# Kernel optimization log

Measured on AMD Instinct MI355X. Metric: run time of the kernel, lower is better.

## Reference

```python
import jax, jax.numpy as jnp
import numpy as np

B, N, C = 4, 4096, 512
K = 683  # ceil(N / ratio=6.0)
TAU = 1.0
W_OCC, W_REP, W_ENT = 1.0, 0.1, 0.01
REP_TOPK, REP_MARGIN = 4, -1.0
NEG = -1e9


def setup_inputs() -> dict:
    key = jax.random.key(0)
    ks = jax.random.split(key, 5)
    s = jax.random.normal(ks[0], (B, N, C), jnp.float32)
    mu = jax.random.normal(ks[1], (B, N, 3), jnp.float32)
    # SPD covariance per residue: L L^T + 0.1 I
    L = jax.random.normal(ks[2], (B, N, 3, 3), jnp.float32) * 0.3
    Sigma = jnp.einsum('bnij,bnkj->bnik', L, L) + 0.1 * jnp.eye(3, dtype=jnp.float32)
    mask = jnp.ones((B, N), jnp.float32)
    W = jax.random.normal(ks[3], (C, C), jnp.float32) / np.sqrt(C).astype(np.float32)
    b = jnp.zeros((C,), jnp.float32)
    slots = jax.random.normal(ks[4], (K, C), jnp.float32) * 0.02
    return {"s": s, "mu": mu, "Sigma": Sigma, "mask": mask, "W": W, "b": b, "slots": slots}


def reference(s, mu, Sigma, mask, W, b, slots):
    Kk = slots.shape[0]
    # A = softmax((Linear(s)) . slots / tau), masked
    s_proj = jnp.einsum('bnc,dc->bnd', s, W) + b            # nn.Linear: x @ W^T + b
    logits = jnp.einsum('bnc,kc->bnk', s_proj, slots) / TAU
    logits = jnp.where((mask < 0.5)[..., None], NEG, logits)
    A = jax.nn.softmax(logits, axis=-1) * mask[..., None]   # [B,N,K]

    denom = jnp.maximum(A.sum(axis=1), 1e-8)                # [B,K]
    s_c = jnp.einsum('bnk,bnc->bkc', A, s) / denom[..., None]

    # moment-matching merge
    w = A / (A.sum(axis=1, keepdims=True) + 1e-8)           # [B,N,K]
    mu_c = jnp.einsum('bnk,bnd->bkd', w, mu)                # [B,K,3]
    intra = jnp.einsum('bnk,bnij->bkij', w, Sigma)          # [B,K,3,3]
    diff = mu[:, :, None, :] - mu_c[:, None, :, :]          # [B,N,K,3]
    inter = jnp.einsum('bnk,bnki,bnkj->bkij', w, diff, diff)
    Sigma_c = intra + inter                                 # [B,K,3,3]

    # occupancy balance loss
    occ = A.sum(axis=1)
    occ = occ / jnp.maximum(occ.sum(axis=-1, keepdims=True), 1e-8)
    loss_occ = jnp.mean((occ - 1.0 / Kk) ** 2)

    # repulsion loss (pairwise Gaussian overlap)
    delta = mu_c[:, :, None, :] - mu_c[:, None, :, :]       # [B,K,K,3]
    sig_sum = Sigma_c[:, :, None] + Sigma_c[:, None, :]     # [B,K,K,3,3]
    inv = jnp.linalg.inv(sig_sum + 1e-6 * jnp.eye(3, dtype=s.dtype))
    dist2 = jnp.einsum('bpqi,bpqij,bpqj->bpq', delta, inv, delta)
    score = -0.5 * dist2
    eye = jnp.eye(Kk, dtype=bool)[None]
    score = jnp.where(eye, NEG, score)
    top = jax.lax.top_k(score, min(REP_TOPK, Kk - 1))[0]
    loss_rep = jnp.mean(jax.nn.relu(top - REP_MARGIN))

    # entropy loss
    Ac = jnp.maximum(A, 1e-8)
    ent = -(Ac * jnp.log(Ac)).sum(axis=-1)                  # [B,N]
    loss_ent = (ent * mask).sum() / jnp.maximum(mask.sum(), 1.0)

    total = W_OCC * loss_occ + W_REP * loss_rep + W_ENT * loss_ent
    return (A, s_c, mu_c, Sigma_c, loss_occ, loss_rep, loss_ent, total)
```

## Files before the change

### kernel.cpp

```cpp
#include <hip/hip_runtime.h>
#include <math.h>

#define B_    4
#define N_    4096
#define C_    512
#define KSLOT 683

using bf16x8 = __attribute__((ext_vector_type(8))) short;
using f32x4  = __attribute__((ext_vector_type(4))) float;

#define OFF_A    0
#define OFF_SC   (B_*N_*KSLOT)
#define OFF_MU   (OFF_SC + B_*KSLOT*C_)
#define OFF_SIG  (OFF_MU + B_*KSLOT*3)
#define OFF_LOSS (OFF_SIG + B_*KSLOT*9)

#define WS_MOM    0
#define WS_INVMAX (WS_MOM + B_*KSLOT*16)
#define WS_OCCTB  (WS_INVMAX + B_*KSLOT)
#define WS_OCCT   (WS_OCCTB + 256)
#define WS_ENTB   (WS_OCCT + 4)
#define WS_MSB    (WS_ENTB + 256)
#define WS_OCCLB  (WS_MSB + 256)
#define WS_REPB   (WS_OCCLB + 256)
#define WS_BS     (WS_REPB + 256)
#define WS_FEND   (WS_BS + 704)

#define US_BASE  (WS_FEND*2)
#define US_SBF   US_BASE
#define US_STF   (US_SBF + B_*N_*C_)
#define US_WSL   (US_STF + B_*C_*N_)
#define US_FT    (US_WSL + 704*C_)
#define US_ATB   (US_FT + B_*16*N_)
#define US_END   (US_ATB + (size_t)B_*768*N_)


__device__ __forceinline__ ushort f2bf(float x) {
  union { float f; unsigned u; } v; v.f = x;
  unsigned r = v.u + 0x7fffu + ((v.u >> 16) & 1u);
  return (ushort)(r >> 16);
}

__device__ __forceinline__ float bf2f(ushort x) {
  union { unsigned u; float f; } v; v.u = ((unsigned)x) << 16;
  return v.f;
}

__device__ __forceinline__ float blockSum256(float v, float* red) {
#pragma unroll
  for (int off = 32; off; off >>= 1) v += __shfl_xor(v, off);
  __syncthreads();
  if ((threadIdx.x & 63) == 0) red[threadIdx.x >> 6] = v;
  __syncthreads();
  return red[0] + red[1] + red[2] + red[3];
}

__device__ __forceinline__ void top4_insert(float v, float& t0, float& t1, float& t2, float& t3) {
  if (v > t3) {
    if (v > t2) {
      t3 = t2;
      if (v > t1) {
        t2 = t1;
        if (v > t0) { t1 = t0; t0 = v; } else t1 = v;
      } else t2 = v;
    } else t3 = v;
  }
}

__global__ __launch_bounds__(256) void prep_all(const float* __restrict__ s,
                                                ushort* __restrict__ sbf,
                                                ushort* __restrict__ stf,
                                                const float* __restrict__ mu,
                                                const float* __restrict__ Sig,
                                                ushort* __restrict__ ftg,
                                                const float* __restrict__ slots,
                                                const float* __restrict__ W,
                                                ushort* __restrict__ wsl,
                                                const float* __restrict__ bvec,
                                                float* __restrict__ bs) {
  __shared__ __align__(16) char PS[16640];
  const int bid = blockIdx.x;
  const int t = threadIdx.x;
  if (bid < 342) {
    float (*SL)[512] = (float(*)[512])PS;
    const int idx = bid;
    const int k0 = (idx % 171) * 4;
    const int c = (idx / 171) * 256 + t;
    for (int id2 = t; id2 < 4 * 512; id2 += 256) {
      int kk = id2 >> 9, d = id2 & 511;
      SL[kk][d] = (k0 + kk < KSLOT) ? slots[(size_t)(k0 + kk) * C_ + d] : 0.f;
    }
    __syncthreads();
    float acc[4];
#pragma unroll
    for (int i = 0; i < 4; ++i) acc[i] = 0.f;
    for (int d0 = 0; d0 < C_; d0 += 8) {
      float wv[8];
#pragma unroll
      for (int j = 0; j < 8; ++j) wv[j] = W[(size_t)(d0 + j) * C_ + c];
#pragma unroll
      for (int j = 0; j < 8; ++j) {
#pragma unroll
        for (int i = 0; i < 4; ++i) acc[i] += SL[i][d0 + j] * wv[j];
      }
    }
#pragma unroll
    for (int i = 0; i < 4; ++i)
      if (k0 + i < KSLOT) wsl[(size_t)(k0 + i) * C_ + c] = f2bf(acc[i]);
  } else if (bid < 513) {
    const int widx = (bid - 342) * 4 + (t >> 6);
    const int lane = t & 63;
    if (widx < KSLOT) {
      const float* srow = slots + (size_t)widx * C_;
      float acc = 0.f;
#pragma unroll
      for (int j = 0; j < 8; ++j) {
        int d = lane + j * 64;
        acc += srow[d] * bvec[d];
      }
#pragma unroll
      for (int off = 32; off; off >>= 1) acc += __shfl_xor(acc, off);
      if (lane == 0) bs[widx] = acc;
    }
  } else if (bid < 577) {
    ushort (*FT)[272] = (ushort(*)[272])PS;
    const int fb = bid - 513;
    const size_t ng = (size_t)fb * 256 + t;
    const float* mp = mu + ng * 3;
    const float* sp = Sig + ng * 9;
    float m0 = mp[0], m1 = mp[1], m2 = mp[2];
    FT[0][t] = 0x3F80;
    FT[1][t] = f2bf(m0); FT[2][t] = f2bf(m1); FT[3][t] = f2bf(m2);
    FT[4][t] = f2bf(m0 * m0); FT[5][t] = f2bf(m0 * m1); FT[6][t] = f2bf(m0 * m2);
    FT[7][t] = f2bf(m1 * m1); FT[8][t] = f2bf(m1 * m2); FT[9][t] = f2bf(m2 * m2);
    FT[10][t] = f2bf(sp[0]); FT[11][t] = f2bf(sp[1]); FT[12][t] = f2bf(sp[2]);
    FT[13][t] = f2bf(sp[4]); FT[14][t] = f2bf(sp[5]); FT[15][t] = f2bf(sp[8]);
    __syncthreads();
    const int b = (int)((fb * 256) >> 12);
    const int n0b = (fb * 256) & (N_ - 1);
    for (int u = t; u < 512; u += 256) {
      int f = u >> 5, off = (u & 31) * 8;
      *(uint4*)(ftg + ((size_t)b * 16 + f) * N_ + n0b + off) = *(uint4*)(&FT[f][off]);
    }
  } else {
    float (*T)[65] = (float(*)[65])PS;
    const int cid = bid - 577;
    const int b = cid >> 9;
    const int rem = cid & 511;
    const int n0 = (rem >> 3) * 64;
    const int c0 = (rem & 7) * 64;
    const int tr = t >> 4;
    const int tc = (t & 15) * 4;
#pragma unroll
    for (int i = 0; i < 4; ++i) {
      const int row = i * 16 + tr;
      float4 v = *(const float4*)(s + ((size_t)(b * N_ + n0 + row)) * C_ + c0 + tc);
      ushort4 u;
      u.x = f2bf(v.x); u.y = f2bf(v.y); u.z = f2bf(v.z); u.w = f2bf(v.w);
      *(ushort4*)(sbf + ((size_t)(b * N_ + n0 + row)) * C_ + c0 + tc) = u;
      T[row][tc + 0] = v.x; T[row][tc + 1] = v.y;
      T[row][tc + 2] = v.z; T[row][tc + 3] = v.w;
    }
    __syncthreads();
#pragma unroll
    for (int i = 0; i < 4; ++i) {
      const int c = i * 16 + tr;
      const int n4 = tc;
      ushort4 o;
      o.x = f2bf(T[n4 + 0][c]); o.y = f2bf(T[n4 + 1][c]);
      o.z = f2bf(T[n4 + 2][c]); o.w = f2bf(T[n4 + 3][c]);
      *(ushort4*)(stf + ((size_t)(b * C_ + c0 + c)) * N_ + n0 + n4) = o;
    }
  }
}

__global__ __launch_bounds__(256) void bs_kernel(const float* __restrict__ slots,
                                                 const float* __restrict__ bvec,
                                                 float* __restrict__ bs) {
  int k = blockIdx.x * 256 + threadIdx.x;
  if (k >= KSLOT) return;
  const float* srow = slots + (size_t)k * C_;
  float acc = 0.f;
  for (int d = 0; d < C_; ++d) acc += srow[d] * bvec[d];
  bs[k] = acc;
}

__device__ __forceinline__ void g1_epilogue(
    f32x4 (&acc)[11], const int rowbase, const int t, const int lane,
    const int rowg, const int colw,
    const float* __restrict__ bs, const float* __restrict__ mask,
    float* __restrict__ Aout, ushort* __restrict__ atb,
    float* __restrict__ entb, float* __restrict__ msb,
    ushort* Af, float (&red4)[32][4], const int binid) {
  __syncthreads();
  int cols[11]; bool valid[11];
#pragma unroll
  for (int cf = 0; cf < 11; ++cf) {
    cols[cf] = colw * 176 + cf * 16 + (lane & 15);
    valid[cf] = (cols[cf] < KSLOT);
    float bv = valid[cf] ? bs[cols[cf]] : 0.f;
#pragma unroll
    for (int r = 0; r < 4; ++r) acc[cf][r] += bv;
  }
  float m4[4];
#pragma unroll
  for (int r = 0; r < 4; ++r) m4[r] = -3.0e38f;
#pragma unroll
  for (int cf = 0; cf < 11; ++cf)
    if (valid[cf]) {
#pragma unroll
      for (int r = 0; r < 4; ++r) m4[r] = fmaxf(m4[r], acc[cf][r]);
    }
#pragma unroll
  for (int off = 1; off < 16; off <<= 1) {
#pragma unroll
    for (int r = 0; r < 4; ++r) m4[r] = fmaxf(m4[r], __shfl_xor(m4[r], off));
  }
  if ((lane & 15) == 0) {
#pragma unroll
    for (int r = 0; r < 4; ++r) red4[rowg * 16 + (lane >> 4) * 4 + r][colw] = m4[r];
  }
  __syncthreads();
#pragma unroll
  for (int r = 0; r < 4; ++r) {
    int rl = rowg * 16 + (lane >> 4) * 4 + r;
    m4[r] = fmaxf(fmaxf(red4[rl][0], red4[rl][1]), fmaxf(red4[rl][2], red4[rl][3]));
  }
  __syncthreads();
  float s4[4] = {0.f, 0.f, 0.f, 0.f};
#pragma unroll
  for (int cf = 0; cf < 11; ++cf)
    if (valid[cf]) {
#pragma unroll
      for (int r = 0; r < 4; ++r) {
        float e = __expf(acc[cf][r] - m4[r]);
        acc[cf][r] = e;
        s4[r] += e;
      }
    }
#pragma unroll
  for (int off = 1; off < 16; off <<= 1) {
#pragma unroll
    for (int r = 0; r < 4; ++r) s4[r] += __shfl_xor(s4[r], off);
  }
  if ((lane & 15) == 0) {
#pragma unroll
    for (int r = 0; r < 4; ++r) red4[rowg * 16 + (lane >> 4) * 4 + r][colw] = s4[r];
  }
  __syncthreads();
  float inv4[4], mr4[4];
#pragma unroll
  for (int r = 0; r < 4; ++r) {
    int rl = rowg * 16 + (lane >> 4) * 4 + r;
    float S = red4[rl][0] + red4[rl][1] + red4[rl][2] + red4[rl][3];
    inv4[r] = 1.f / S;
    mr4[r] = mask[rowbase + rl];
  }
  __syncthreads();
  float ent4[4] = {0.f, 0.f, 0.f, 0.f};
#pragma unroll
  for (int cf = 0; cf < 11; ++cf)
    if (valid[cf]) {
#pragma unroll
      for (int r = 0; r < 4; ++r) {
        int rl = rowg * 16 + (lane >> 4) * 4 + r;
        float a = acc[cf][r] * inv4[r] * mr4[r];
        Af[rl * KSLOT + cols[cf]] = f2bf(a);
        float ac = fmaxf(a, 1e-8f);
        ent4[r] -= ac * __logf(ac);
      }
    }
#pragma unroll
  for (int off = 1; off < 16; off <<= 1) {
#pragma unroll
    for (int r = 0; r < 4; ++r) ent4[r] += __shfl_xor(ent4[r], off);
  }
  if ((lane & 15) == 0) {
#pragma unroll
    for (int r = 0; r < 4; ++r) red4[rowg * 16 + (lane >> 4) * 4 + r][colw] = ent4[r];
  }
  __syncthreads();
  if (t < 64) {
    float er = 0.f, ms = 0.f;
    if (t < 32) {
      float e = red4[t][0] + red4[t][1] + red4[t][2] + red4[t][3];
      float m = mask[rowbase + t];
      er = e * m; ms = m;
    }
#pragma unroll
    for (int off = 32; off; off >>= 1) { er += __shfl_xor(er, off); ms += __shfl_xor(ms, off); }
    if (t == 0) {
      atomicAdd(&entb[binid], er);
      atomicAdd(&msb[binid], ms);
    }
  }
  float* Ag = Aout + (size_t)rowbase * KSLOT;
  for (int i = t; i < (32 * KSLOT) / 4; i += 512) {
    ushort4 u4 = *(const ushort4*)(Af + i * 4);
    float4 v;
    v.x = bf2f(u4.x); v.y = bf2f(u4.y); v.z = bf2f(u4.z); v.w = bf2f(u4.w);
    *(float4*)(Ag + i * 4) = v;
  }
  {
    const int bb = rowbase >> 12;
    const int n0b = rowbase & (N_ - 1);
    ushort* Atb = atb + ((size_t)bb * 768) * N_ + n0b;
    for (int u = t; u < KSLOT * 4; u += 512) {
      int k = u >> 2, q = u & 3;
      ushort tmp[8];
#pragma unroll
      for (int j = 0; j < 8; ++j) tmp[j] = Af[(q * 8 + j) * KSLOT + k];
      *(uint4*)(Atb + (size_t)k * N_ + q * 8) = *(uint4*)tmp;
    }
  }
}

__global__ __launch_bounds__(512)
void gemm1sm(const ushort* __restrict__ sbf,
             const ushort* __restrict__ wsl,
             const float* __restrict__ bs,
             const float* __restrict__ mask,
             float* __restrict__ Aout,
             ushort* __restrict__ atb,
             float* __restrict__ entb,
             float* __restrict__ msb) {
  __shared__ __align__(16) char SMEM[49152];
  __shared__ float red4[32][4];
  const int t = threadIdx.x;
  const int lane = t & 63;
  const int w = t >> 6;
  const int rowg = w >> 2;
  const int colw = w & 3;
  const int row0 = blockIdx.x * 64;
  const int r16 = rowg * 16 + (lane & 15);

  const ushort* arow0 = sbf + (size_t)(row0 + r16) * C_ + (lane >> 4) * 8;
  const ushort* arow1 = arow0 + (size_t)32 * C_;
  bf16x8 g0 = *(const bf16x8*)(arow0);
  bf16x8 g1 = *(const bf16x8*)(arow1);
  bf16x8 p0, p1;

  f32x4 acc0[11], acc1[11];
  f32x4 zero = {0.f, 0.f, 0.f, 0.f};
#pragma unroll
  for (int cf = 0; cf < 11; ++cf) { acc0[cf] = zero; acc1[cf] = zero; }

  const int ach = (lane >> 4);
#pragma unroll
  for (int slab = 0; slab < 16; ++slab) {
    if (slab) __syncthreads();
#pragma unroll
    for (int i = 0; i < 6; ++i) {
      int idx = t + i * 512;
      int r = idx >> 2;
      int chs = (idx & 3) ^ (r & 3);
      const ushort* g = wsl + (size_t)r * C_ + slab * 32 + chs * 8;
      char* l = (char*)SMEM + (t & 448) * 16 + i * 8192;
      __builtin_amdgcn_global_load_lds(
          (const __attribute__((address_space(1))) void*)g,
          (__attribute__((address_space(3))) void*)l, 16, 0, 0);
    }
    __syncthreads();
    if (slab < 15) {
      p0 = *(const bf16x8*)(arow0 + (slab + 1) * 32);
      p1 = *(const bf16x8*)(arow1 + (slab + 1) * 32);
    }
#pragma unroll
    for (int cf = 0; cf < 11; ++cf) {
      int br = colw * 176 + cf * 16 + (lane & 15);
      bf16x8 bf = *(const bf16x8*)(SMEM + br * 64 + ((ach * 16) ^ ((br & 3) << 4)));
      acc0[cf] = __builtin_amdgcn_mfma_f32_16x16x32_bf16(g0, bf, acc0[cf], 0, 0, 0);
      acc1[cf] = __builtin_amdgcn_mfma_f32_16x16x32_bf16(g1, bf, acc1[cf], 0, 0, 0);
    }
    g0 = p0; g1 = p1;
  }

  ushort* Af = (ushort*)SMEM;
  g1_epilogue(acc0, row0, t, lane, rowg, colw, bs, mask, Aout, atb, entb, msb,
              Af, red4, (blockIdx.x * 2) & 255);
  g1_epilogue(acc1, row0 + 32, t, lane, rowg, colw, bs, mask, Aout, atb, entb, msb,
              Af, red4, (blockIdx.x * 2 + 1) & 255);
}

#define G2BUFB 18432
__global__ __launch_bounds__(256) void gemm2t(const ushort* __restrict__ atb,
                                              const ushort* __restrict__ stf,
                                              const ushort* __restrict__ ftg,
                                              float* __restrict__ sc,
                                              float* __restrict__ MOM) {
  __shared__ __align__(16) char LB[2 * G2BUFB];
  const int t = threadIdx.x;
  const int lane = t & 63;
  const int w = t >> 6;
  const int wm = w >> 1;
  const int wn = w & 1;
  const int fhw = blockIdx.x;
  const int logical = (fhw & 7) * 44 + (fhw >> 3);
  const int kt = logical % 11;
  const int ct = (logical / 11) & 7;
  const int b  = logical / 88;
  const bool do_mom = (ct == 0);
  const ushort* Ab = atb + ((size_t)b * 768 + kt * 64) * N_;
  const ushort* Sb = stf + ((size_t)b * C_ + ct * 64) * N_;
  const ushort* Fb = ftg + ((size_t)b * 16) * N_;

  f32x4 zero = {0.f, 0.f, 0.f, 0.f};
  f32x4 acc[2][2];
#pragma unroll
  for (int i = 0; i < 2; ++i)
#pragma unroll
    for (int j = 0; j < 2; ++j) acc[i][j] = zero;
  f32x4 accf[2];
#pragma unroll
  for (int i = 0; i < 2; ++i) accf[i] = zero;

#define G2_STAGE(BUFI, NB)                                                   \
  {                                                                          \
    char* AtL = LB + (BUFI) * G2BUFB;                                        \
    char* SsL = AtL + 8192;                                                  \
    char* FtL = AtL + 16384;                                                 \
    _Pragma("unroll")                                                        \
    for (int i = 0; i < 2; ++i) {                                            \
      int idx = t + i * 256;                                                 \
      int r = idx >> 3;                                                      \
      int chs = (idx & 7) ^ (r & 7);                                         \
      const ushort* g = Ab + (size_t)r * N_ + (NB) + chs * 8;                \
      char* l = AtL + i * 4096 + (t & 192) * 16;                             \
      __builtin_amdgcn_global_load_lds(                                      \
          (const __attribute__((address_space(1))) void*)g,                  \
          (__attribute__((address_space(3))) void*)l, 16, 0, 0);             \
    }                                                                        \
    _Pragma("unroll")                                                        \
    for (int i = 0; i < 2; ++i) {                                            \
      int idx = t + i * 256;                                                 \
      int r = idx >> 3;                                                      \
      int chs = (idx & 7) ^ (r & 7);                                         \
      const ushort* g = Sb + (size_t)r * N_ + (NB) + chs * 8;                \
      char* l = SsL + i * 4096 + (t & 192) * 16;                             \
      __builtin_amdgcn_global_load_lds(                                      \
          (const __attribute__((address_space(1))) void*)g,                  \
          (__attribute__((address_space(3))) void*)l, 16, 0, 0);             \
    }                                                                        \
    if (do_mom && t < 128) {                                                 \
      int idx = t;                                                           \
      int r = idx >> 3;                                                      \
      int chs = (idx & 7) ^ (r & 7);                                         \
      const ushort* g = Fb + (size_t)r * N_ + (NB) + chs * 8;                \
      char* l = FtL + (t & 192) * 16;                                       \
      __builtin_amdgcn_global_load_lds(                                      \
          (const __attribute__((address_space(1))) void*)g,                  \
          (__attribute__((address_space(3))) void*)l, 16, 0, 0);             \
    }                                                                        \
  }

  G2_STAGE(0, 0)
  for (int st = 0; st < 64; ++st) {
    const int cur = st & 1;
    __syncthreads();
    if (st < 63) G2_STAGE(cur ^ 1, (st + 1) * 64)
    char* AtL = LB + cur * G2BUFB;
    char* SsL = AtL + 8192;
    char* FtL = AtL + 16384;
#pragma unroll
    for (int ks2 = 0; ks2 < 2; ++ks2) {
      const int ach = ks2 * 4 + (lane >> 4);
      bf16x8 afr[2], bfr[2];
#pragma unroll
      for (int kf = 0; kf < 2; ++kf) {
        int ar = wm * 32 + kf * 16 + (lane & 15);
        afr[kf] = *(const bf16x8*)(AtL + ar * 128 + ((ach * 16) ^ ((ar & 7) << 4)));
      }
#pragma unroll
      for (int cg = 0; cg < 2; ++cg) {
        int br = wn * 32 + cg * 16 + (lane & 15);
        bfr[cg] = *(const bf16x8*)(SsL + br * 128 + ((ach * 16) ^ ((br & 7) << 4)));
      }
#pragma unroll
      for (int kf = 0; kf < 2; ++kf)
#pragma unroll
        for (int cg = 0; cg < 2; ++cg)
          acc[kf][cg] = __builtin_amdgcn_mfma_f32_16x16x32_bf16(afr[kf], bfr[cg], acc[kf][cg], 0, 0, 0);
      if (do_mom && wn == 0) {
        int fr = lane & 15;
        bf16x8 ffr = *(const bf16x8*)(FtL + fr * 128 + ((ach * 16) ^ ((fr & 7) << 4)));
#pragma unroll
        for (int kf = 0; kf < 2; ++kf)
          accf[kf] = __builtin_amdgcn_mfma_f32_16x16x32_bf16(afr[kf], ffr, accf[kf], 0, 0, 0);
      }
    }
  }
#undef G2_STAGE

#pragma unroll
  for (int kf = 0; kf < 2; ++kf) {
#pragma unroll
    for (int r = 0; r < 4; ++r) {
      int k = kt * 64 + wm * 32 + kf * 16 + (lane >> 4) * 4 + r;
      if (k >= KSLOT) continue;
      float* dst = sc + ((size_t)(b * KSLOT + k)) * C_ + ct * 64 + wn * 32;
#pragma unroll
      for (int cg = 0; cg < 2; ++cg)
        dst[cg * 16 + (lane & 15)] = acc[kf][cg][r];
    }
  }
  if (do_mom && wn == 0) {
#pragma unroll
    for (int kf = 0; kf < 2; ++kf) {
#pragma unroll
      for (int r = 0; r < 4; ++r) {
        int k = kt * 64 + wm * 32 + kf * 16 + (lane >> 4) * 4 + r;
        if (k >= KSLOT) continue;
        MOM[((size_t)b * KSLOT + k) * 16 + (lane & 15)] = accf[kf][r];
      }
    }
  }
}

__global__ __launch_bounds__(128) void scale_sc(float* __restrict__ sc,
                                                const float* __restrict__ invmax) {
  const int bk = blockIdx.x;
  const float sv = invmax[bk];
  float4* p = (float4*)(sc + (size_t)bk * C_);
  int t = threadIdx.x;
  float4 v = p[t];
  v.x *= sv; v.y *= sv; v.z *= sv; v.w *= sv;
  p[t] = v;
}

__global__ __launch_bounds__(256) void moments_kernel(const float* __restrict__ Amat,
                                                      const float* __restrict__ mu,
                                                      const float* __restrict__ Sig,
                                                      float* __restrict__ MOM) {
  __shared__ float red[64][17];
  const int b = blockIdx.z;
  const int kx = threadIdx.x & 63;
  const int k = blockIdx.x * 64 + kx;
  const int ng = threadIdx.x >> 6;
  const int n0 = blockIdx.y * 128;
  const bool valid = (k < KSLOT);

  float acc[16];
#pragma unroll
  for (int i = 0; i < 16; ++i) acc[i] = 0.f;

  const float* Abase = Amat + (size_t)b * N_ * KSLOT + k;
  const float* mubase = mu + ((size_t)b * N_) * 3;
  const float* sgbase = Sig + ((size_t)b * N_) * 9;

  for (int j = 0; j < 32; ++j) {
    const int n = n0 + ng + j * 4;
    float a = valid ? Abase[(size_t)n * KSLOT] : 0.f;
    const float* mp = mubase + (size_t)n * 3;
    const float* sp = sgbase + (size_t)n * 9;
    float m0 = mp[0], m1 = mp[1], m2 = mp[2];
    acc[0] += a;
    acc[1] += a * m0; acc[2] += a * m1; acc[3] += a * m2;
    acc[4] += a * m0 * m0; acc[5] += a * m0 * m1; acc[6] += a * m0 * m2;
    acc[7] += a * m1 * m1; acc[8] += a * m1 * m2; acc[9] += a * m2 * m2;
    acc[10] += a * sp[0]; acc[11] += a * sp[1]; acc[12] += a * sp[2];
    acc[13] += a * sp[4]; acc[14] += a * sp[5]; acc[15] += a * sp[8];
  }

  if (ng == 0) {
#pragma unroll
    for (int i = 0; i < 16; ++i) red[kx][i] = acc[i];
  }
  __syncthreads();
  if (ng == 1) {
#pragma unroll
    for (int i = 0; i < 16; ++i) red[kx][i] += acc[i];
  }
  __syncthreads();
  if (ng == 2) {
#pragma unroll
    for (int i = 0; i < 16; ++i) red[kx][i] += acc[i];
  }
  __syncthreads();
  if (ng == 3) {
#pragma unroll
    for (int i = 0; i < 16; ++i) red[kx][i] += acc[i];
  }
  __syncthreads();
  if (ng == 0 && valid) {
    float* dst = MOM + ((size_t)b * KSLOT + k) * 16;
#pragma unroll
    for (int i = 0; i < 16; ++i) atomicAdd(&dst[i], red[kx][i]);
  }
}

__global__ __launch_bounds__(256) void finalize_bk(const float* __restrict__ MOM,
                                                   float* __restrict__ muc,
                                                   float* __restrict__ sigc,
                                                   float* __restrict__ invmax,
                                                   float* __restrict__ occtb) {
  int bk = blockIdx.x * 256 + threadIdx.x;
  if (bk >= B_ * KSLOT) return;
  int b = bk / KSLOT;
  const float* T = MOM + (size_t)bk * 16;
  float den = T[0];
  float inv_eps = 1.f / (den + 1e-8f);
  float inv_mx = 1.f / fmaxf(den, 1e-8f);
  float mc0 = T[1] * inv_eps, mc1 = T[2] * inv_eps, mc2 = T[3] * inv_eps;
  float M0 = den * inv_eps;
  float cf = 2.f - M0;
  float S00 = (T[10] + T[4]) * inv_eps - cf * mc0 * mc0;
  float S01 = (T[11] + T[5]) * inv_eps - cf * mc0 * mc1;
  float S02 = (T[12] + T[6]) * inv_eps - cf * mc0 * mc2;
  float S11 = (T[13] + T[7]) * inv_eps - cf * mc1 * mc1;
  float S12 = (T[14] + T[8]) * inv_eps - cf * mc1 * mc2;
  float S22 = (T[15] + T[9]) * inv_eps - cf * mc2 * mc2;
  muc[(size_t)bk * 3 + 0] = mc0;
  muc[(size_t)bk * 3 + 1] = mc1;
  muc[(size_t)bk * 3 + 2] = mc2;
  float* sg = sigc + (size_t)bk * 9;
  sg[0] = S00; sg[1] = S01; sg[2] = S02;
  sg[3] = S01; sg[4] = S11; sg[5] = S12;
  sg[6] = S02; sg[7] = S12; sg[8] = S22;
  invmax[bk] = inv_mx;
  atomicAdd(&occtb[b * 64 + (threadIdx.x & 63)], den);
}

__global__ __launch_bounds__(256) void occ_loss_kernel(const float* __restrict__ MOM,
                                                       const float* __restrict__ occtb,
                                                       float* __restrict__ occlb) {
  __shared__ float red[4];
  __shared__ float occT[4];
  int tid = threadIdx.x;
  {
    float v = occtb[tid];
#pragma unroll
    for (int off = 32; off; off >>= 1) v += __shfl_xor(v, off);
    if ((tid & 63) == 0) occT[tid >> 6] = v;
  }
  __syncthreads();
  int bk = blockIdx.x * 256 + tid;
  float d2 = 0.f;
  if (bk < B_ * KSLOT) {
    int b = bk / KSLOT;
    float den = MOM[(size_t)bk * 16];
    float occ = den / fmaxf(occT[b], 1e-8f);
    float d = occ - (1.f / (float)KSLOT);
    d2 = d * d;
  }
  float ssum = blockSum256(d2, red);
  if (tid == 0) occlb[blockIdx.x] = ssum;
}

__global__ __launch_bounds__(256) void repulsion_kernel2(const float* __restrict__ muc,
                                                         const float* __restrict__ sigc,
                                                         float* __restrict__ repb) {
  __shared__ float L[KSLOT * 13];
  const int b = blockIdx.y;
  const int t = threadIdx.x;
  const float* mb = muc + (size_t)b * KSLOT * 3;
  const float* sb = sigc + (size_t)b * KSLOT * 9;
  for (int idx = t; idx < KSLOT * 3; idx += 256) {
    int r = idx / 3, c = idx - r * 3;
    L[r * 13 + c] = mb[idx];
  }
  for (int idx = t; idx < KSLOT * 9; idx += 256) {
    int r = idx / 9, c = idx - r * 9;
    L[r * 13 + 3 + c] = sb[idx];
  }
  __syncthreads();
  const int w = t >> 6, lane = t & 63;
  const int p = blockIdx.x * 4 + w;
  if (p >= KSLOT) return;
  const float* Lp = L + p * 13;
  const float mp0 = Lp[0], mp1 = Lp[1], mp2 = Lp[2];
  const float pa = Lp[3], pb = Lp[4], pc = Lp[5], pd = Lp[7], pe = Lp[8], pf = Lp[11];
  float t0 = -3e38f, t1 = -3e38f, t2 = -3e38f, t3 = -3e38f;
  for (int q = lane; q < KSLOT; q += 64) {
    if (q == p) continue;
    const float* Lq = L + q * 13;
    float d0 = mp0 - Lq[0];
    float d1 = mp1 - Lq[1];
    float d2 = mp2 - Lq[2];
    float a  = pa + Lq[3] + 1e-6f;
    float bb = pb + Lq[4];
    float cc = pc + Lq[5];
    float d  = pd + Lq[7] + 1e-6f;
    float e  = pe + Lq[8];
    float f  = pf + Lq[11] + 1e-6f;
    float C00 = d * f - e * e;
    float C01 = cc * e - bb * f;
    float C02 = bb * e - cc * d;
    float C11 = a * f - cc * cc;
    float C12 = bb * cc - a * e;
    float C22 = a * d - bb * bb;
    float det = a * C00 + bb * C01 + cc * C02;
    float dist2 = (C00 * d0 * d0 + C11 * d1 * d1 + C22 * d2 * d2 +
                   2.f * (C01 * d0 * d1 + C02 * d0 * d2 + C12 * d1 * d2)) / det;
    top4_insert(-0.5f * dist2, t0, t1, t2, t3);
  }
#pragma unroll
  for (int off = 1; off < 64; off <<= 1) {
    float u0 = __shfl_xor(t0, off);
    float u1 = __shfl_xor(t1, off);
    float u2 = __shfl_xor(t2, off);
    float u3 = __shfl_xor(t3, off);
    top4_insert(u0, t0, t1, t2, t3);
    top4_insert(u1, t0, t1, t2, t3);
    top4_insert(u2, t0, t1, t2, t3);
    top4_insert(u3, t0, t1, t2, t3);
  }
  if (lane == 0) {
    float s = fmaxf(t0 + 1.f, 0.f) + fmaxf(t1 + 1.f, 0.f) +
              fmaxf(t2 + 1.f, 0.f) + fmaxf(t3 + 1.f, 0.f);
    atomicAdd(&repb[(b * KSLOT + p) & 255], s);
  }
}

__global__ __launch_bounds__(256) void final_scalars(const float* __restrict__ entb,
                                                     const float* __restrict__ msb,
                                                     const float* __restrict__ occlb,
                                                     const float* __restrict__ repb,
                                                     float* __restrict__ out) {
  __shared__ float red[4];
  int tid = threadIdx.x;
  float e = blockSum256(entb[tid], red);
  float ms = blockSum256(msb[tid], red);
  float oc = blockSum256(occlb[tid], red);
  float rp = blockSum256(repb[tid], red);
  if (tid == 0) {
    float loss_ent = e / fmaxf(ms, 1.f);
    float loss_occ = oc / (float)(B_ * KSLOT);
    float loss_rep = rp / (float)(B_ * KSLOT * 4);
    out[0] = loss_occ;
    out[1] = loss_rep;
    out[2] = loss_ent;
    out[3] = 1.0f * loss_occ + 0.1f * loss_rep + 0.01f * loss_ent;
  }
}


__global__ __launch_bounds__(256) void wslots_kernel(const float* __restrict__ slots,
                                                     const float* __restrict__ W,
                                                     float* __restrict__ Wsl) {
  int k = blockIdx.x;
  int c = blockIdx.y * 256 + threadIdx.x;
  const float* srow = slots + (size_t)k * C_;
  float acc = 0.f;
  for (int d = 0; d < C_; d += 4) {
    acc += srow[d] * W[(size_t)d * C_ + c];
    acc += srow[d + 1] * W[(size_t)(d + 1) * C_ + c];
    acc += srow[d + 2] * W[(size_t)(d + 2) * C_ + c];
    acc += srow[d + 3] * W[(size_t)(d + 3) * C_ + c];
  }
  Wsl[(size_t)k * C_ + c] = acc;
}

__global__ __launch_bounds__(256) void softmax_rows(float* __restrict__ Amat,
                                                    const float* __restrict__ mask,
                                                    float* __restrict__ entb,
                                                    float* __restrict__ msb) {
  __shared__ float red[4];
  const int row = blockIdx.x;
  const int tid = threadIdx.x;
  float* rowp = Amat + (size_t)row * KSLOT;
  const float m = mask[row];
  const bool msk = (m < 0.5f);
  float v[3];
#pragma unroll
  for (int i = 0; i < 3; ++i) {
    int k = tid + i * 256;
    if (k < KSLOT) {
      float l = rowp[k];
      v[i] = msk ? -1e9f : l;
    } else v[i] = -3.0e38f;
  }
  float lmax = fmaxf(fmaxf(v[0], v[1]), v[2]);
#pragma unroll
  for (int off = 32; off; off >>= 1) lmax = fmaxf(lmax, __shfl_xor(lmax, off));
  __syncthreads();
  if ((tid & 63) == 0) red[tid >> 6] = lmax;
  __syncthreads();
  lmax = fmaxf(fmaxf(red[0], red[1]), fmaxf(red[2], red[3]));
  float lsum = 0.f;
#pragma unroll
  for (int i = 0; i < 3; ++i) {
    int k = tid + i * 256;
    float e = (k < KSLOT) ? expf(v[i] - lmax) : 0.f;
    v[i] = e;
    lsum += e;
  }
  lsum = blockSum256(lsum, red);
  float inv = 1.f / lsum;
  float ent = 0.f;
#pragma unroll
  for (int i = 0; i < 3; ++i) {
    int k = tid + i * 256;
    if (k < KSLOT) {
      float a = v[i] * inv * m;
      rowp[k] = a;
      float ac = fmaxf(a, 1e-8f);
      ent -= ac * logf(ac);
    }
  }
  ent = blockSum256(ent, red);
  if (tid == 0) {
    int bin = blockIdx.x & 255;
    atomicAdd(&entb[bin], ent * m);
    atomicAdd(&msb[bin], m);
  }
}

__global__ __launch_bounds__(256) void gemm_nt(const float* __restrict__ Am,
                                               const float* __restrict__ Bm,
                                               const float* __restrict__ bias,
                                               float* __restrict__ Cm,
                                               int M, int Nout, int Kd,
                                               int lda, int ldb, int ldc) {
  __shared__ float As[16][132];
  __shared__ float Bs[16][132];
  const int tid = threadIdx.x;
  const int tx = tid & 15, ty = tid >> 4;
  const int m0 = blockIdx.x * 128, n0 = blockIdx.y * 128;
  float acc[8][8];
#pragma unroll
  for (int i = 0; i < 8; ++i)
#pragma unroll
    for (int j = 0; j < 8; ++j) acc[i][j] = 0.f;
  const int r = tid >> 1, hc = (tid & 1) * 8;
  for (int k0 = 0; k0 < Kd; k0 += 16) {
    float va[8], vb[8];
    int gm = m0 + r;
    if (gm < M) {
      const float* p = Am + (size_t)gm * lda + k0 + hc;
      *(float4*)(va) = *(const float4*)(p);
      *(float4*)(va + 4) = *(const float4*)(p + 4);
    } else {
#pragma unroll
      for (int i = 0; i < 8; ++i) va[i] = 0.f;
    }
    int gn = n0 + r;
    if (gn < Nout) {
      const float* p = Bm + (size_t)gn * ldb + k0 + hc;
      *(float4*)(vb) = *(const float4*)(p);
      *(float4*)(vb + 4) = *(const float4*)(p + 4);
    } else {
#pragma unroll
      for (int i = 0; i < 8; ++i) vb[i] = 0.f;
    }
#pragma unroll
    for (int i = 0; i < 8; ++i) As[hc + i][r] = va[i];
#pragma unroll
    for (int i = 0; i < 8; ++i) Bs[hc + i][r] = vb[i];
    __syncthreads();
#pragma unroll
    for (int kk = 0; kk < 16; ++kk) {
      float a[8], bb[8];
      *(float4*)(a) = *(const float4*)&As[kk][ty * 8];
      *(float4*)(a + 4) = *(const float4*)&As[kk][ty * 8 + 4];
      *(float4*)(bb) = *(const float4*)&Bs[kk][tx * 8];
      *(float4*)(bb + 4) = *(const float4*)&Bs[kk][tx * 8 + 4];
#pragma unroll
      for (int i = 0; i < 8; ++i)
#pragma unroll
        for (int j = 0; j < 8; ++j) acc[i][j] += a[i] * bb[j];
    }
    __syncthreads();
  }
#pragma unroll
  for (int i = 0; i < 8; ++i) {
    int gm = m0 + ty * 8 + i;
    if (gm >= M) continue;
    float* crow = Cm + (size_t)gm * ldc;
#pragma unroll
    for (int j = 0; j < 8; ++j) {
      int gn = n0 + tx * 8 + j;
      if (gn < Nout) crow[gn] = acc[i][j] + bias[gn];
    }
  }
}

__global__ __launch_bounds__(256) void gemm_tn(const float* __restrict__ Aall,
                                               const float* __restrict__ Ball,
                                               const float* __restrict__ scale,
                                               float* __restrict__ Call) {
  const int b = blockIdx.z;
  const float* Am = Aall + (size_t)b * N_ * KSLOT;
  const float* Bv = Ball + (size_t)b * N_ * C_;
  float* Cm = Call + (size_t)b * KSLOT * C_;
  const float* sc = scale + (size_t)b * KSLOT;
  __shared__ float As[16][132];
  __shared__ float Bs[16][68];
  const int tid = threadIdx.x;
  const int tx = tid & 15, ty = tid >> 4;
  const int m0 = blockIdx.x * 128, n0 = blockIdx.y * 64;
  float acc[8][4];
#pragma unroll
  for (int i = 0; i < 8; ++i)
#pragma unroll
    for (int j = 0; j < 4; ++j) acc[i][j] = 0.f;
  const int rr = tid >> 4;
  const int mq = tid & 15;
  const int cq = (tid & 15) * 4;
  for (int r0 = 0; r0 < N_; r0 += 16) {
#pragma unroll
    for (int i = 0; i < 8; ++i) {
      int mm = mq + 16 * i;
      int gm = m0 + mm;
      As[rr][mm] = (gm < KSLOT) ? Am[(size_t)(r0 + rr) * KSLOT + gm] : 0.f;
    }
    *(float4*)&Bs[rr][cq] = *(const float4*)(Bv + (size_t)(r0 + rr) * C_ + n0 + cq);
    __syncthreads();
#pragma unroll
    for (int kk = 0; kk < 16; ++kk) {
      float a[8], bb[4];
      *(float4*)(a) = *(const float4*)&As[kk][ty * 8];
      *(float4*)(a + 4) = *(const float4*)&As[kk][ty * 8 + 4];
      *(float4*)(bb) = *(const float4*)&Bs[kk][tx * 4];
#pragma unroll
      for (int i = 0; i < 8; ++i)
#pragma unroll
        for (int j = 0; j < 4; ++j) acc[i][j] += a[i] * bb[j];
    }
    __syncthreads();
  }
#pragma unroll
  for (int i = 0; i < 8; ++i) {
    int gm = m0 + ty * 8 + i;
    if (gm < KSLOT) {
      float s = sc[gm];
      float4 v;
      v.x = acc[i][0] * s; v.y = acc[i][1] * s; v.z = acc[i][2] * s; v.w = acc[i][3] * s;
      *(float4*)(Cm + (size_t)gm * C_ + n0 + tx * 4) = v;
    }
  }
}

extern "C" void kernel_launch(void* const* d_in, const int* in_sizes, int n_in,
                              void* d_out, int out_size, void* d_ws, size_t ws_size,
                              hipStream_t stream) {
  const float* s     = (const float*)d_in[0];
  const float* mu    = (const float*)d_in[1];
  const float* Sig   = (const float*)d_in[2];
  const float* mask  = (const float*)d_in[3];
  const float* W     = (const float*)d_in[4];
  const float* bvec  = (const float*)d_in[5];
  const float* slots = (const float*)d_in[6];
  float* out = (float*)d_out;
  float* ws  = (float*)d_ws;

  float* Amat = out + OFF_A;
  const bool fast = (ws_size >= (size_t)US_END * 2 + 64);

  (void)hipMemsetAsync(ws, 0, WS_FEND * sizeof(float), stream);

  if (fast) {
    ushort* usw = (ushort*)ws;
    ushort* sbf = usw + US_SBF;
    ushort* stf = usw + US_STF;
    ushort* wsl = usw + US_WSL;
    ushort* ftg = usw + US_FT;
    ushort* atb = usw + US_ATB;

    prep_all<<<dim3(2625), 256, 0, stream>>>(
        s, sbf, stf, mu, Sig, ftg, slots, W, wsl, bvec, ws + WS_BS);

    gemm1sm<<<dim3(B_ * N_ / 64), 512, 0, stream>>>(
        sbf, wsl, ws + WS_BS, mask, Amat, atb, ws + WS_ENTB, ws + WS_MSB);

    gemm2t<<<dim3(352), 256, 0, stream>>>(
        atb, stf, ftg, out + OFF_SC, ws + WS_MOM);

    finalize_bk<<<dim3((B_ * KSLOT + 255) / 256), 256, 0, stream>>>(
        ws + WS_MOM, out + OFF_MU, out + OFF_SIG, ws + WS_INVMAX, ws + WS_OCCTB);

    occ_loss_kernel<<<dim3((B_ * KSLOT + 255) / 256), 256, 0, stream>>>(
        ws + WS_MOM, ws + WS_OCCTB, ws + WS_OCCLB);

    scale_sc<<<dim3(B_ * KSLOT), 128, 0, stream>>>(out + OFF_SC, ws + WS_INVMAX);

    repulsion_kernel2<<<dim3((KSLOT + 3) / 4, B_), 256, 0, stream>>>(
        out + OFF_MU, out + OFF_SIG, ws + WS_REPB);

    final_scalars<<<dim3(1), 256, 0, stream>>>(
        ws + WS_ENTB, ws + WS_MSB, ws + WS_OCCLB, ws + WS_REPB, out + OFF_LOSS);
  } else {
    float* Wsl = out + OFF_SC;

    bs_kernel<<<dim3(3), 256, 0, stream>>>(slots, bvec, ws + WS_BS);
    wslots_kernel<<<dim3(KSLOT, 2), 256, 0, stream>>>(slots, W, Wsl);
    gemm_nt<<<dim3((B_ * N_) / 128, (KSLOT + 127) / 128), 256, 0, stream>>>(
        s, Wsl, ws + WS_BS, Amat, B_ * N_, KSLOT, C_, C_, C_, KSLOT);
    softmax_rows<<<dim3(B_ * N_), 256, 0, stream>>>(Amat, mask, ws + WS_ENTB, ws + WS_MSB);
    moments_kernel<<<dim3(11, N_ / 128, B_), 256, 0, stream>>>(
        Amat, mu, Sig, ws + WS_MOM);
    finalize_bk<<<dim3((B_ * KSLOT + 255) / 256), 256, 0, stream>>>(
        ws + WS_MOM, out + OFF_MU, out + OFF_SIG, ws + WS_INVMAX, ws + WS_OCCTB);
    occ_loss_kernel<<<dim3((B_ * KSLOT + 255) / 256), 256, 0, stream>>>(
        ws + WS_MOM, ws + WS_OCCTB, ws + WS_OCCLB);
    gemm_tn<<<dim3((KSLOT + 127) / 128, C_ / 64, B_), 256, 0, stream>>>(
        Amat, s, ws + WS_INVMAX, out + OFF_SC);
    repulsion_kernel2<<<dim3((KSLOT + 3) / 4, B_), 256, 0, stream>>>(
        out + OFF_MU, out + OFF_SIG, ws + WS_REPB);
    final_scalars<<<dim3(1), 256, 0, stream>>>(
        ws + WS_ENTB, ws + WS_MSB, ws + WS_OCCLB, ws + WS_REPB, out + OFF_LOSS);
  }
}
```

Baseline: 164.2 us.

## Load GEMM1 slot operands directly from global memory instead of LDS staging

The slot-matrix GEMM in the fused softmax kernel stops staging the weight tile through shared memory with global_load_lds and per-slab barriers. Each wave now reads its B fragments straight from global (L2/L1-cached) memory and processes two 32-wide K chunks per iteration, with no __syncthreads in the main loop. The shared buffer shrinks to just what the epilogue needs. The trade is that each wave issues many more global loads of the small, heavily reused slot matrix and loses explicit prefetching, so latency hiding depends on the cache and the compiler's scheduling.

```diff
diff --git a/kernel.cpp b/kernel.cpp
--- a/kernel.cpp
+++ b/kernel.cpp
@@ -191,7 +191,7 @@
     const float* __restrict__ bs, const float* __restrict__ mask,
     float* __restrict__ Aout, ushort* __restrict__ atb,
     float* __restrict__ entb, float* __restrict__ msb,
-    ushort* Af, float (&red4)[32][4], const int binid) {
+    ushort* Af, float (&red4)[32][4], const int binid, const int nthreads) {
   __syncthreads();
   int cols[11]; bool valid[11];
 #pragma unroll
@@ -295,7 +295,7 @@
     }
   }
   float* Ag = Aout + (size_t)rowbase * KSLOT;
-  for (int i = t; i < (32 * KSLOT) / 4; i += 512) {
+  for (int i = t; i < (32 * KSLOT) / 4; i += nthreads) {
     ushort4 u4 = *(const ushort4*)(Af + i * 4);
     float4 v;
     v.x = bf2f(u4.x); v.y = bf2f(u4.y); v.z = bf2f(u4.z); v.w = bf2f(u4.w);
@@ -305,7 +305,7 @@
     const int bb = rowbase >> 12;
     const int n0b = rowbase & (N_ - 1);
     ushort* Atb = atb + ((size_t)bb * 768) * N_ + n0b;
-    for (int u = t; u < KSLOT * 4; u += 512) {
+    for (int u = t; u < KSLOT * 4; u += nthreads) {
       int k = u >> 2, q = u & 3;
       ushort tmp[8];
 #pragma unroll
@@ -324,7 +324,7 @@
              ushort* __restrict__ atb,
              float* __restrict__ entb,
              float* __restrict__ msb) {
-  __shared__ __align__(16) char SMEM[49152];
+  __shared__ __align__(16) char SMEM[43776];
   __shared__ float red4[32][4];
   const int t = threadIdx.x;
   const int lane = t & 63;
@@ -336,50 +336,36 @@
 
   const ushort* arow0 = sbf + (size_t)(row0 + r16) * C_ + (lane >> 4) * 8;
   const ushort* arow1 = arow0 + (size_t)32 * C_;
-  bf16x8 g0 = *(const bf16x8*)(arow0);
-  bf16x8 g1 = *(const bf16x8*)(arow1);
-  bf16x8 p0, p1;
+  const ushort* bbase = wsl + (size_t)(colw * 176 + (lane & 15)) * C_ + (lane >> 4) * 8;
 
   f32x4 acc0[11], acc1[11];
   f32x4 zero = {0.f, 0.f, 0.f, 0.f};
 #pragma unroll
   for (int cf = 0; cf < 11; ++cf) { acc0[cf] = zero; acc1[cf] = zero; }
 
-  const int ach = (lane >> 4);
-#pragma unroll
-  for (int slab = 0; slab < 16; ++slab) {
-    if (slab) __syncthreads();
-#pragma unroll
-    for (int i = 0; i < 6; ++i) {
-      int idx = t + i * 512;
-      int r = idx >> 2;
-      int chs = (idx & 3) ^ (r & 3);
-      const ushort* g = wsl + (size_t)r * C_ + slab * 32 + chs * 8;
-      char* l = (char*)SMEM + (t & 448) * 16 + i * 8192;
-      __builtin_amdgcn_global_load_lds(
-          (const __attribute__((address_space(1))) void*)g,
-          (__attribute__((address_space(3))) void*)l, 16, 0, 0);
-    }
-    __syncthreads();
-    if (slab < 15) {
-      p0 = *(const bf16x8*)(arow0 + (slab + 1) * 32);
-      p1 = *(const bf16x8*)(arow1 + (slab + 1) * 32);
-    }
+#pragma unroll
+  for (int slab = 0; slab < 8; ++slab) {
+    bf16x8 g0a = *(const bf16x8*)(arow0 + slab * 64);
+    bf16x8 g0b = *(const bf16x8*)(arow0 + slab * 64 + 32);
+    bf16x8 g1a = *(const bf16x8*)(arow1 + slab * 64);
+    bf16x8 g1b = *(const bf16x8*)(arow1 + slab * 64 + 32);
 #pragma unroll
     for (int cf = 0; cf < 11; ++cf) {
-      int br = colw * 176 + cf * 16 + (lane & 15);
-      bf16x8 bf = *(const bf16x8*)(SMEM + br * 64 + ((ach * 16) ^ ((br & 3) << 4)));
-      acc0[cf] = __builtin_amdgcn_mfma_f32_16x16x32_bf16(g0, bf, acc0[cf], 0, 0, 0);
-      acc1[cf] = __builtin_amdgcn_mfma_f32_16x16x32_bf16(g1, bf, acc1[cf], 0, 0, 0);
-    }
-    g0 = p0; g1 = p1;
+      const ushort* bp = bbase + (size_t)cf * 16 * C_ + slab * 64;
+      bf16x8 b0 = *(const bf16x8*)(bp);
+      bf16x8 b1 = *(const bf16x8*)(bp + 32);
+      acc0[cf] = __builtin_amdgcn_mfma_f32_16x16x32_bf16(g0a, b0, acc0[cf], 0, 0, 0);
+      acc1[cf] = __builtin_amdgcn_mfma_f32_16x16x32_bf16(g1a, b0, acc1[cf], 0, 0, 0);
+      acc0[cf] = __builtin_amdgcn_mfma_f32_16x16x32_bf16(g0b, b1, acc0[cf], 0, 0, 0);
+      acc1[cf] = __builtin_amdgcn_mfma_f32_16x16x32_bf16(g1b, b1, acc1[cf], 0, 0, 0);
+    }
   }
 
   ushort* Af = (ushort*)SMEM;
   g1_epilogue(acc0, row0, t, lane, rowg, colw, bs, mask, Aout, atb, entb, msb,
-              Af, red4, (blockIdx.x * 2) & 255);
+              Af, red4, (blockIdx.x * 2) & 255, 512);
   g1_epilogue(acc1, row0 + 32, t, lane, rowg, colw, bs, mask, Aout, atb, entb, msb,
-              Af, red4, (blockIdx.x * 2 + 1) & 255);
+              Af, red4, (blockIdx.x * 2 + 1) & 255, 512);
 }
 
 #define G2BUFB 18432
```

Result: slower. 189.8 us (+15.6%).
